# Optimization experiments

Hardware: AMD Instinct MI355X
Metric: run time of the kernel (lower is better)

The kernel has to match this reference:

```python
import jax, jax.numpy as jnp
import numpy as np

ACT_GUARD = 2.0   # 2 ** act_guard_bit (act_guard_bit = 1)
WGT_GUARD = 2.0   # 2 ** weight_guard_bit (weight_guard_bit = 1)


def _ste_round(v):
    # straight-through estimator round (QNMethod.STE)
    return v + jax.lax.stop_gradient(jnp.round(v) - v)


def setup_inputs() -> dict:
    key = jax.random.key(0)
    k_x, k_w, k_b = jax.random.split(key, 3)
    B, S, DIN, DOUT = 4, 2048, 2048, 8192
    ACT_INIT_S, ACT_INIT_Q, LOG_S_INIT = -10.0, 10.0, -8.0
    x = jax.random.normal(k_x, (B, S, DIN), dtype=jnp.float32)
    weight = jax.random.normal(k_w, (DOUT, DIN), dtype=jnp.float32) * 0.02
    bias = jax.random.normal(k_b, (DOUT,), dtype=jnp.float32) * 0.01
    log_act_s = jnp.full((1,), ACT_INIT_S, dtype=jnp.float32)
    log_act_q = jnp.full((1,), ACT_INIT_Q, dtype=jnp.float32)
    act_b = jnp.full((1,), -jnp.exp2(ACT_INIT_Q - 1.0), dtype=jnp.float32)  # -512
    log_wght_s = jnp.full((DOUT, 1), LOG_S_INIT, dtype=jnp.float32)
    return {"x": x, "weight": weight, "bias": bias, "log_act_s": log_act_s,
            "log_act_q": log_act_q, "act_b": act_b, "log_wght_s": log_wght_s}


def reference(x, weight, bias, log_act_s, log_act_q, act_b, log_wght_s):
    # --- activation fake-quant (per-tensor) ---
    s = jnp.exp2(log_act_s)                       # [1]
    q = jnp.exp2(log_act_q)                       # [1]
    zp = jnp.round(act_b / s * ACT_GUARD) / ACT_GUARD * s  # guard-bit rounded zero point
    lo, hi = zp, zp + q - s
    qx = _ste_round((jnp.clip(x, lo, hi) - zp) / s)
    x_dq = qx * s + zp                            # dequantized activations

    # --- weight fake-quant (per-channel over out dim, amin/amax over dim 1) ---
    w_scale = jnp.exp2(log_wght_s)                # [DOUT, 1]
    wmin = jnp.min(weight, axis=1, keepdims=True)
    wmax = jnp.max(weight, axis=1, keepdims=True)
    qwmin = jnp.round(wmin / w_scale * WGT_GUARD) / WGT_GUARD * w_scale
    qwmax = jnp.round(wmax / w_scale * WGT_GUARD) / WGT_GUARD * w_scale
    qw = _ste_round((jnp.clip(weight, qwmin, qwmax) - qwmin) / w_scale)
    w_dq = qw * w_scale + qwmin                   # dequantized weights

    # --- affine: y = x @ W.T + b ---
    return jnp.einsum('bsi,oi->bso', x_dq, w_dq) + bias
```

## Files before the change

kernel.cpp:

```cpp
#include <hip/hip_runtime.h>
#include <hip/hip_bf16.h>


using f16x8 = __attribute__((ext_vector_type(8))) _Float16;
using f32x4 = __attribute__((ext_vector_type(4))) float;

#define AS1 __attribute__((address_space(1)))
#define AS3 __attribute__((address_space(3)))

static __device__ __forceinline__ void gload_lds16(const void* g, void* l) {
    __builtin_amdgcn_global_load_lds((const AS1 void*)g, (AS3 void*)l, 16, 0, 0);
}

__global__ __launch_bounds__(256) void wquant_kernel(
    const float* __restrict__ W, const float* __restrict__ lws,
    _Float16* __restrict__ Wq) {
    constexpr int K = 2048;
    const int row = blockIdx.x;
    const int t = threadIdx.x;
    const float* w = W + (size_t)row * K;

    float4 v0 = ((const float4*)w)[t * 2];
    float4 v1 = ((const float4*)w)[t * 2 + 1];
    float vals[8] = {v0.x, v0.y, v0.z, v0.w, v1.x, v1.y, v1.z, v1.w};

    float mn = vals[0], mx = vals[0];
#pragma unroll
    for (int i = 1; i < 8; ++i) {
        mn = fminf(mn, vals[i]);
        mx = fmaxf(mx, vals[i]);
    }
#pragma unroll
    for (int off = 32; off >= 1; off >>= 1) {
        mn = fminf(mn, __shfl_xor(mn, off));
        mx = fmaxf(mx, __shfl_xor(mx, off));
    }
    __shared__ float smn[4], smx[4];
    if ((t & 63) == 0) { smn[t >> 6] = mn; smx[t >> 6] = mx; }
    __syncthreads();
    mn = fminf(fminf(smn[0], smn[1]), fminf(smn[2], smn[3]));
    mx = fmaxf(fmaxf(smx[0], smx[1]), fmaxf(smx[2], smx[3]));

    const float l = lws[row];
    const float ws = exp2f(l);
    const float rs = exp2f(-l);
    const float qwmin = rintf(mn * rs * 2.0f) * 0.5f * ws;
    const float qwmax = rintf(mx * rs * 2.0f) * 0.5f * ws;

    f16x8 out;
#pragma unroll
    for (int i = 0; i < 8; ++i) {
        float c = fminf(fmaxf(vals[i], qwmin), qwmax);
        float qw = rintf((c - qwmin) * rs);
        out[i] = (_Float16)(qw * ws + qwmin);
    }
    *(f16x8*)&Wq[(size_t)row * K + (size_t)t * 8] = out;
}

__global__ __launch_bounds__(256) void xquant_kernel(
    const float* __restrict__ X,
    const float* __restrict__ las, const float* __restrict__ laq,
    const float* __restrict__ ab, _Float16* __restrict__ Xq) {
    const float ls = las[0], lq = laq[0];
    const float s = exp2f(ls);
    const float rs = exp2f(-ls);
    const float q = exp2f(lq);
    const float zp = rintf(ab[0] * rs * 2.0f) * 0.5f * s;
    const float lo = zp;
    const float hi = (zp + q) - s;

    const size_t base = ((size_t)blockIdx.x * 256 + threadIdx.x) * 8;
    float4 v0 = *(const float4*)&X[base];
    float4 v1 = *(const float4*)&X[base + 4];
    float vals[8] = {v0.x, v0.y, v0.z, v0.w, v1.x, v1.y, v1.z, v1.w};

    f16x8 out;
#pragma unroll
    for (int i = 0; i < 8; ++i) {
        float c = fminf(fmaxf(vals[i], lo), hi);
        float qx = rintf((c - zp) * rs);
        out[i] = (_Float16)(qx * s + zp);
    }
    *(f16x8*)&Xq[base] = out;
}

__global__ __launch_bounds__(512, 2) void gemm_kernel(
    const _Float16* __restrict__ A, const _Float16* __restrict__ B,
    const float* __restrict__ bias, float* __restrict__ C) {
    constexpr int N = 8192, K = 2048;
    constexpr int KT = K / 64;
    constexpr int NBN = N / 256;

    __shared__ char smem[131072];

    const int bid = blockIdx.x;
    const int cpx = gridDim.x >> 3;
    const int swzb = (bid & 7) * cpx + (bid >> 3);
    const int bm = swzb / NBN;
    const int bn = swzb % NBN;

    const int t = threadIdx.x;
    const int lane = t & 63;
    const int wid = t >> 6;
    const int wr = wid >> 2;
    const int wc = wid & 3;
    const int l15 = lane & 15;
    const int lq = lane >> 4;

    const int d0 = t * 16, d1 = d0 + 8192;
    const int r0 = d0 >> 7, c0 = (((d0 & 127) ^ (((d0 >> 7) & 7) << 4)) >> 1);
    const int r1 = d1 >> 7, c1 = (((d1 & 127) ^ (((d1 >> 7) & 7) << 4)) >> 1);
    const _Float16* Agb = A + (size_t)bm * 256 * K;
    const _Float16* Bgb = B + (size_t)bn * 256 * K;

    const int cp0 = (lq * 16) ^ ((l15 & 7) << 4);
    const int cp1 = cp0 ^ 64;

    f32x4 acc[8][4] = {};
    f16x8 fA[8][2], fB[4][2];

#define STAGEH(GB, RO, DBS, H, KS) do {                                        \
        const _Float16* _g = (GB) + (size_t)((H) * 128) * K + (size_t)(KS) * 64;\
        char* _l = smem + (RO) + ((DBS) * 2 + (H)) * 16384;                    \
        gload_lds16(_g + (size_t)r0 * K + c0, _l + d0);                        \
        gload_lds16(_g + (size_t)r1 * K + c1, _l + d1);                        \
    } while (0)

#define STAGET(DBS, KS) do {                                                   \
        STAGEH(Agb, 0,     DBS, 0, KS);                                        \
        STAGEH(Agb, 0,     DBS, 1, KS);                                        \
        STAGEH(Bgb, 65536, DBS, 0, KS);                                        \
        STAGEH(Bgb, 65536, DBS, 1, KS);                                        \
    } while (0)

#define VMC(NN) asm volatile("s_waitcnt vmcnt(" #NN ")" ::: "memory")
#define BAR()   __builtin_amdgcn_s_barrier()
#define PRIO(P) __builtin_amdgcn_s_setprio(P)

    STAGET(0, 0);
    VMC(0);
    BAR();

    for (int kt = 0; kt < KT; ++kt) {
        const int db = kt & 1;
        const int nx = (kt + 1 < KT) ? kt + 1 : KT - 1;

        STAGET(db ^ 1, nx);

        const char* _a = smem + (db * 2 + wr) * 16384 + l15 * 128;
        const char* _b = smem + 65536 + (db * 2 + (wc >> 1)) * 16384 +
                         (wc & 1) * 8192 + l15 * 128;
#pragma unroll
        for (int m = 0; m < 8; ++m)
            fA[m][0] = *(const f16x8*)(_a + m * 2048 + cp0);
#pragma unroll
        for (int n = 0; n < 4; ++n)
            fB[n][0] = *(const f16x8*)(_b + n * 2048 + cp0);
#pragma unroll
        for (int m = 0; m < 8; ++m)
            fA[m][1] = *(const f16x8*)(_a + m * 2048 + cp1);
#pragma unroll
        for (int n = 0; n < 4; ++n)
            fB[n][1] = *(const f16x8*)(_b + n * 2048 + cp1);

        asm volatile("s_waitcnt lgkmcnt(12)" ::: "memory");
        __builtin_amdgcn_sched_barrier(0);
        PRIO(1);
#pragma unroll
        for (int m = 0; m < 8; ++m)
#pragma unroll
            for (int n = 0; n < 4; ++n)
                acc[m][n] = __builtin_amdgcn_mfma_f32_16x16x32_f16(
                    fA[m][0], fB[n][0], acc[m][n], 0, 0, 0);
        PRIO(0);

        asm volatile("s_waitcnt lgkmcnt(0)" ::: "memory");
        __builtin_amdgcn_sched_barrier(0);
        PRIO(1);
#pragma unroll
        for (int m = 0; m < 8; ++m)
#pragma unroll
            for (int n = 0; n < 4; ++n)
                acc[m][n] = __builtin_amdgcn_mfma_f32_16x16x32_f16(
                    fA[m][1], fB[n][1], acc[m][n], 0, 0, 0);
        PRIO(0);

        VMC(0);
        BAR();
    }
#undef STAGEH
#undef STAGET
#undef VMC
#undef BAR
#undef PRIO

#pragma unroll
    for (int m = 0; m < 8; ++m) {
        const int row = bm * 256 + wr * 128 + m * 16 + lq * 4;
#pragma unroll
        for (int n = 0; n < 4; ++n) {
            const int col = bn * 256 + wc * 64 + n * 16 + l15;
            const float bv = bias[col];
#pragma unroll
            for (int r = 0; r < 4; ++r) {
                C[(size_t)(row + r) * N + col] = acc[m][n][r] + bv;
            }
        }
    }
}

extern "C" void kernel_launch(void* const* d_in, const int* in_sizes, int n_in,
                              void* d_out, int out_size, void* d_ws, size_t ws_size,
                              hipStream_t stream) {
    const float* x    = (const float*)d_in[0];
    const float* w    = (const float*)d_in[1];
    const float* bias = (const float*)d_in[2];
    const float* las  = (const float*)d_in[3];
    const float* laq  = (const float*)d_in[4];
    const float* ab   = (const float*)d_in[5];
    const float* lws  = (const float*)d_in[6];
    float* out = (float*)d_out;

    constexpr size_t MK = (size_t)8192 * 2048;
    _Float16* xq = (_Float16*)d_ws;
    _Float16* wq = (_Float16*)((char*)d_ws + MK * sizeof(_Float16));

    xquant_kernel<<<8192, 256, 0, stream>>>(x, las, laq, ab, xq);
    wquant_kernel<<<8192, 256, 0, stream>>>(w, lws, wq);
    gemm_kernel<<<1024, 512, 0, stream>>>(xq, wq, bias, out);
}
```

Measured before the change: 304.9 us.

## Fuse activation and weight quant kernels, rework GEMM block swizzle, drop manual waits

Combines the activation and weight fake-quant kernels into a single launch, dispatched by block index, to remove one launch and let both run concurrently. Changes the GEMM block-to-tile mapping so each XCD group covers a compact band of M tiles across all N tiles, aiming for better L2 reuse. Removes hand-placed lgkmcnt waits, sched barriers and priority hints in the MFMA loop, leaving scheduling to the compiler, which may lose overlap of LDS reads with MFMAs.

```diff
diff --git a/kernel.cpp b/kernel.cpp
--- a/kernel.cpp
+++ b/kernel.cpp
@@ -12,76 +12,77 @@
     __builtin_amdgcn_global_load_lds((const AS1 void*)g, (AS3 void*)l, 16, 0, 0);
 }
 
-__global__ __launch_bounds__(256) void wquant_kernel(
-    const float* __restrict__ W, const float* __restrict__ lws,
-    _Float16* __restrict__ Wq) {
-    constexpr int K = 2048;
-    const int row = blockIdx.x;
-    const int t = threadIdx.x;
-    const float* w = W + (size_t)row * K;
-
-    float4 v0 = ((const float4*)w)[t * 2];
-    float4 v1 = ((const float4*)w)[t * 2 + 1];
-    float vals[8] = {v0.x, v0.y, v0.z, v0.w, v1.x, v1.y, v1.z, v1.w};
-
-    float mn = vals[0], mx = vals[0];
-#pragma unroll
-    for (int i = 1; i < 8; ++i) {
-        mn = fminf(mn, vals[i]);
-        mx = fmaxf(mx, vals[i]);
-    }
-#pragma unroll
-    for (int off = 32; off >= 1; off >>= 1) {
-        mn = fminf(mn, __shfl_xor(mn, off));
-        mx = fmaxf(mx, __shfl_xor(mx, off));
-    }
-    __shared__ float smn[4], smx[4];
-    if ((t & 63) == 0) { smn[t >> 6] = mn; smx[t >> 6] = mx; }
-    __syncthreads();
-    mn = fminf(fminf(smn[0], smn[1]), fminf(smn[2], smn[3]));
-    mx = fmaxf(fmaxf(smx[0], smx[1]), fmaxf(smx[2], smx[3]));
-
-    const float l = lws[row];
-    const float ws = exp2f(l);
-    const float rs = exp2f(-l);
-    const float qwmin = rintf(mn * rs * 2.0f) * 0.5f * ws;
-    const float qwmax = rintf(mx * rs * 2.0f) * 0.5f * ws;
-
-    f16x8 out;
-#pragma unroll
-    for (int i = 0; i < 8; ++i) {
-        float c = fminf(fmaxf(vals[i], qwmin), qwmax);
-        float qw = rintf((c - qwmin) * rs);
-        out[i] = (_Float16)(qw * ws + qwmin);
-    }
-    *(f16x8*)&Wq[(size_t)row * K + (size_t)t * 8] = out;
-}
-
-__global__ __launch_bounds__(256) void xquant_kernel(
+__global__ __launch_bounds__(256) void quant_kernel(
     const float* __restrict__ X,
     const float* __restrict__ las, const float* __restrict__ laq,
-    const float* __restrict__ ab, _Float16* __restrict__ Xq) {
-    const float ls = las[0], lq = laq[0];
-    const float s = exp2f(ls);
-    const float rs = exp2f(-ls);
-    const float q = exp2f(lq);
-    const float zp = rintf(ab[0] * rs * 2.0f) * 0.5f * s;
-    const float lo = zp;
-    const float hi = (zp + q) - s;
-
-    const size_t base = ((size_t)blockIdx.x * 256 + threadIdx.x) * 8;
-    float4 v0 = *(const float4*)&X[base];
-    float4 v1 = *(const float4*)&X[base + 4];
-    float vals[8] = {v0.x, v0.y, v0.z, v0.w, v1.x, v1.y, v1.z, v1.w};
-
-    f16x8 out;
-#pragma unroll
-    for (int i = 0; i < 8; ++i) {
-        float c = fminf(fmaxf(vals[i], lo), hi);
-        float qx = rintf((c - zp) * rs);
-        out[i] = (_Float16)(qx * s + zp);
+    const float* __restrict__ ab,
+    const float* __restrict__ W, const float* __restrict__ lws,
+    _Float16* __restrict__ Xq, _Float16* __restrict__ Wq) {
+    constexpr int K = 2048;
+    __shared__ float smn[4], smx[4];
+    const int t = threadIdx.x;
+
+    if (blockIdx.x < 8192) {
+        const float ls = las[0], lq = laq[0];
+        const float s = exp2f(ls);
+        const float rs = exp2f(-ls);
+        const float q = exp2f(lq);
+        const float zp = rintf(ab[0] * rs * 2.0f) * 0.5f * s;
+        const float lo = zp;
+        const float hi = (zp + q) - s;
+
+        const size_t base = ((size_t)blockIdx.x * 256 + t) * 8;
+        float4 v0 = *(const float4*)&X[base];
+        float4 v1 = *(const float4*)&X[base + 4];
+        float vals[8] = {v0.x, v0.y, v0.z, v0.w, v1.x, v1.y, v1.z, v1.w};
+
+        f16x8 out;
+#pragma unroll
+        for (int i = 0; i < 8; ++i) {
+            float c = fminf(fmaxf(vals[i], lo), hi);
+            float qx = rintf((c - zp) * rs);
+            out[i] = (_Float16)(qx * s + zp);
+        }
+        *(f16x8*)&Xq[base] = out;
+    } else {
+        const int row = blockIdx.x - 8192;
+        const float* w = W + (size_t)row * K;
+
+        float4 v0 = ((const float4*)w)[t * 2];
+        float4 v1 = ((const float4*)w)[t * 2 + 1];
+        float vals[8] = {v0.x, v0.y, v0.z, v0.w, v1.x, v1.y, v1.z, v1.w};
+
+        float mn = vals[0], mx = vals[0];
+#pragma unroll
+        for (int i = 1; i < 8; ++i) {
+            mn = fminf(mn, vals[i]);
+            mx = fmaxf(mx, vals[i]);
+        }
+#pragma unroll
+        for (int off = 32; off >= 1; off >>= 1) {
+            mn = fminf(mn, __shfl_xor(mn, off));
+            mx = fmaxf(mx, __shfl_xor(mx, off));
+        }
+        if ((t & 63) == 0) { smn[t >> 6] = mn; smx[t >> 6] = mx; }
+        __syncthreads();
+        mn = fminf(fminf(smn[0], smn[1]), fminf(smn[2], smn[3]));
+        mx = fmaxf(fmaxf(smx[0], smx[1]), fmaxf(smx[2], smx[3]));
+
+        const float l = lws[row];
+        const float ws = exp2f(l);
+        const float rs = exp2f(-l);
+        const float qwmin = rintf(mn * rs * 2.0f) * 0.5f * ws;
+        const float qwmax = rintf(mx * rs * 2.0f) * 0.5f * ws;
+
+        f16x8 out;
+#pragma unroll
+        for (int i = 0; i < 8; ++i) {
+            float c = fminf(fmaxf(vals[i], qwmin), qwmax);
+            float qw = rintf((c - qwmin) * rs);
+            out[i] = (_Float16)(qw * ws + qwmin);
+        }
+        *(f16x8*)&Wq[(size_t)row * K + (size_t)t * 8] = out;
     }
-    *(f16x8*)&Xq[base] = out;
 }
 
 __global__ __launch_bounds__(512, 2) void gemm_kernel(
@@ -89,15 +90,12 @@
     const float* __restrict__ bias, float* __restrict__ C) {
     constexpr int N = 8192, K = 2048;
     constexpr int KT = K / 64;
-    constexpr int NBN = N / 256;
-
     __shared__ char smem[131072];
 
     const int bid = blockIdx.x;
-    const int cpx = gridDim.x >> 3;
-    const int swzb = (bid & 7) * cpx + (bid >> 3);
-    const int bm = swzb / NBN;
-    const int bn = swzb % NBN;
+    const int j = bid >> 3;
+    const int bm = (bid & 7) * 4 + (j & 3);
+    const int bn = j >> 2;
 
     const int t = threadIdx.x;
     const int lane = t & 63;
@@ -133,13 +131,9 @@
         STAGEH(Bgb, 65536, DBS, 1, KS);                                        \
     } while (0)
 
-#define VMC(NN) asm volatile("s_waitcnt vmcnt(" #NN ")" ::: "memory")
-#define BAR()   __builtin_amdgcn_s_barrier()
-#define PRIO(P) __builtin_amdgcn_s_setprio(P)
-
     STAGET(0, 0);
-    VMC(0);
-    BAR();
+    asm volatile("s_waitcnt vmcnt(0)" ::: "memory");
+    __builtin_amdgcn_s_barrier();
 
     for (int kt = 0; kt < KT; ++kt) {
         const int db = kt & 1;
@@ -163,36 +157,24 @@
         for (int n = 0; n < 4; ++n)
             fB[n][1] = *(const f16x8*)(_b + n * 2048 + cp1);
 
-        asm volatile("s_waitcnt lgkmcnt(12)" ::: "memory");
-        __builtin_amdgcn_sched_barrier(0);
-        PRIO(1);
 #pragma unroll
         for (int m = 0; m < 8; ++m)
 #pragma unroll
             for (int n = 0; n < 4; ++n)
                 acc[m][n] = __builtin_amdgcn_mfma_f32_16x16x32_f16(
                     fA[m][0], fB[n][0], acc[m][n], 0, 0, 0);
-        PRIO(0);
-
-        asm volatile("s_waitcnt lgkmcnt(0)" ::: "memory");
-        __builtin_amdgcn_sched_barrier(0);
-        PRIO(1);
 #pragma unroll
         for (int m = 0; m < 8; ++m)
 #pragma unroll
             for (int n = 0; n < 4; ++n)
                 acc[m][n] = __builtin_amdgcn_mfma_f32_16x16x32_f16(
                     fA[m][1], fB[n][1], acc[m][n], 0, 0, 0);
-        PRIO(0);
-
-        VMC(0);
-        BAR();
+
+        asm volatile("s_waitcnt vmcnt(0)" ::: "memory");
+        __builtin_amdgcn_s_barrier();
     }
 #undef STAGEH
 #undef STAGET
-#undef VMC
-#undef BAR
-#undef PRIO
 
 #pragma unroll
     for (int m = 0; m < 8; ++m) {
@@ -225,7 +207,6 @@
     _Float16* xq = (_Float16*)d_ws;
     _Float16* wq = (_Float16*)((char*)d_ws + MK * sizeof(_Float16));
 
-    xquant_kernel<<<8192, 256, 0, stream>>>(x, las, laq, ab, xq);
-    wquant_kernel<<<8192, 256, 0, stream>>>(w, lws, wq);
+    quant_kernel<<<16384, 256, 0, stream>>>(x, las, laq, ab, w, lws, xq, wq);
     gemm_kernel<<<1024, 512, 0, stream>>>(xq, wq, bias, out);
 }
```

After: 279.0 us. 1.09x faster.
